# Optimization experiments

Hardware: AMD Instinct MI355X
Metric: run time of the kernel (lower is better)

The kernel has to match this reference:

```python
import jax, jax.numpy as jnp
import numpy as np

HEADS = 16
HIDDEN = 1024
DH = HIDDEN // HEADS
EPS = 1e-6


def setup_inputs() -> dict:
    key = jax.random.key(0)
    ks = jax.random.split(key, 18)
    B, S, D, H = 8, 4096, HIDDEN, HEADS
    std = 0.02
    inp = {
        "x": jax.random.normal(ks[0], (B, S, D), dtype=jnp.float32),
        "mask": jnp.zeros((B, 1, S), dtype=jnp.float32),
        "Wq": std * jax.random.normal(ks[1], (D, D), dtype=jnp.float32),
        "bq": jnp.zeros((D,), jnp.float32),
        "Wk": std * jax.random.normal(ks[2], (D, D), dtype=jnp.float32),
        "bk": jnp.zeros((D,), jnp.float32),
        "Wv": std * jax.random.normal(ks[3], (D, D), dtype=jnp.float32),
        "bv": jnp.zeros((D,), jnp.float32),
        "Wa": std * jax.random.normal(ks[4], (D, H), dtype=jnp.float32),
        "ba": jnp.zeros((H,), jnp.float32),
        "Wb": std * jax.random.normal(ks[5], (D, H), dtype=jnp.float32),
        "bb": jnp.zeros((H,), jnp.float32),
        "Wu": std * jax.random.normal(ks[6], (D, D), dtype=jnp.float32),
        "bu": jnp.zeros((D,), jnp.float32),
        "Wo": std * jax.random.normal(ks[7], (D, D), dtype=jnp.float32),
        "bo": jnp.zeros((D,), jnp.float32),
        "ln_g": jnp.ones((D,), jnp.float32),
        "ln_b": jnp.zeros((D,), jnp.float32),
    }
    return inp


def reference(x, mask, Wq, bq, Wk, bk, Wv, bv, Wa, ba, Wb, bb, Wu, bu, Wo, bo, ln_g, ln_b):
    B, S, D = x.shape
    H, dh = HEADS, D // HEADS
    scale = (D / H) ** -0.5

    q = x @ Wq + bq  # [B,S,D]
    k = x @ Wk + bk
    v = x @ Wv + bv

    # alpha pooling of q
    ascore = jnp.swapaxes((q @ Wa + ba) * scale, 1, 2) + mask  # [B,H,S]
    aw = jax.nn.softmax(ascore, axis=-1)
    qh = q.reshape(B, S, H, dh)
    q_av = jnp.einsum("bhs,bshd->bhd", aw, qh).reshape(B, 1, D)  # global query

    p = k * q_av  # [B,S,D], broadcast over seq

    # beta pooling of p
    bscore = jnp.swapaxes((p @ Wb + bb) * scale, 1, 2) + mask  # [B,H,S]
    bw = jax.nn.softmax(bscore, axis=-1)
    ph = p.reshape(B, S, H, dh)
    p_av = jnp.einsum("bhs,bshd->bhd", bw, ph).reshape(B, 1, D)  # global key

    u = p_av * v  # [B,S,D]
    r = u @ Wu + bu
    attn_out = (r + q) @ Wo + bo

    y = x + attn_out  # residual (dropout is identity at inference)
    mu = jnp.mean(y, axis=-1, keepdims=True)
    var = jnp.mean(jnp.square(y - mu), axis=-1, keepdims=True)
    return (y - mu) * jax.lax.rsqrt(var + EPS) * ln_g + ln_b
```

## Files before the change

kernel.cpp:

```cpp
#include <hip/hip_runtime.h>

typedef unsigned short u16;
typedef __bf16 bf16x8 __attribute__((ext_vector_type(8)));
typedef float  f32x4  __attribute__((ext_vector_type(4)));

__device__ __forceinline__ float b2f(u16 u) {
    unsigned int v = ((unsigned int)u) << 16;
    return __builtin_bit_cast(float, v);
}
__device__ __forceinline__ u16 f2b(float f) {
    unsigned int v = __builtin_bit_cast(unsigned int, f);
    v += 0x7fffu + ((v >> 16) & 1u);
    return (u16)(v >> 16);
}

#define GLD16(gp, lp) __builtin_amdgcn_global_load_lds( \
    (const __attribute__((address_space(1))) void*)(gp), \
    (__attribute__((address_space(3))) void*)(lp), 16, 0, 0)


__global__ __launch_bounds__(256) void convert_x(const float* __restrict__ x,
                                                 u16* __restrict__ xb) {
    size_t i = ((size_t)blockIdx.x * 256 + threadIdx.x) * 8;
    float4 v0 = *(const float4*)(x + i);
    float4 v1 = *(const float4*)(x + i + 4);
    ushort4 o0, o1;
    o0.x = f2b(v0.x); o0.y = f2b(v0.y); o0.z = f2b(v0.z); o0.w = f2b(v0.w);
    o1.x = f2b(v1.x); o1.y = f2b(v1.y); o1.z = f2b(v1.z); o1.w = f2b(v1.w);
    *(ushort4*)(xb + i)     = o0;
    *(ushort4*)(xb + i + 4) = o1;
}

__global__ __launch_bounds__(256)
void prep_all(const float* __restrict__ Wq, const float* __restrict__ Wk,
              const float* __restrict__ Wv, const float* __restrict__ Wo,
              u16* __restrict__ Wqkvt, u16* __restrict__ Wot,
              const float* __restrict__ Wa, u16* __restrict__ Wat,
              const float* __restrict__ bq, const float* __restrict__ bk,
              const float* __restrict__ bv, float* __restrict__ biasq) {
    __shared__ float tile[64][65];
    int blk = blockIdx.x;
    int tid = threadIdx.x;
    if (blk < 1024) {
        int g = blk >> 8;
        int lb = blk & 255;
        const float* W = (g == 0) ? Wq : (g == 1) ? Wk : (g == 2) ? Wv : Wo;
        u16* Wt = (g == 3) ? Wot : (Wqkvt + (size_t)g * 1048576);
        int kt = (lb & 15) * 64;
        int nt = (lb >> 4) * 64;
        int r = tid >> 4, c4 = (tid & 15) * 4;
        #pragma unroll
        for (int p = 0; p < 4; ++p) {
            int k = kt + p * 16 + r;
            float4 v = *(const float4*)(W + (size_t)k * 1024 + nt + c4);
            tile[c4 + 0][p * 16 + r] = v.x;
            tile[c4 + 1][p * 16 + r] = v.y;
            tile[c4 + 2][p * 16 + r] = v.z;
            tile[c4 + 3][p * 16 + r] = v.w;
        }
        __syncthreads();
        #pragma unroll
        for (int p = 0; p < 4; ++p) {
            int nl = p * 16 + r;
            ushort4 o;
            o.x = f2b(tile[nl][c4 + 0]); o.y = f2b(tile[nl][c4 + 1]);
            o.z = f2b(tile[nl][c4 + 2]); o.w = f2b(tile[nl][c4 + 3]);
            *(ushort4*)(Wt + (size_t)(nt + nl) * 1024 + kt + c4) = o;
        }
    } else if (blk < 1088) {
        int idx = (blk - 1024) * 256 + tid;
        int h = idx >> 10, k = idx & 1023;
        Wat[idx] = f2b(Wa[(k << 4) + h]);
    } else {
        int i = (blk - 1088) * 256 + tid;
        biasq[i] = (i < 1024) ? bq[i] : (i < 2048 ? bk[i - 1024] : bv[i - 2048]);
    }
}

__global__ __launch_bounds__(256) void wu_prime(const float* __restrict__ Wu,
                                                const float* __restrict__ p_av,
                                                u16* __restrict__ Wut) {
    __shared__ float tile[64][65];
    int kt = (blockIdx.x & 15) * 64;
    int nt = (blockIdx.x >> 4) * 64;
    int tid = threadIdx.x;
    int r = tid >> 4, c4 = (tid & 15) * 4;
    #pragma unroll
    for (int p = 0; p < 4; ++p) {
        int k = kt + p * 16 + r;
        float4 v = *(const float4*)(Wu + (size_t)k * 1024 + nt + c4);
        tile[c4 + 0][p * 16 + r] = v.x;
        tile[c4 + 1][p * 16 + r] = v.y;
        tile[c4 + 2][p * 16 + r] = v.z;
        tile[c4 + 3][p * 16 + r] = v.w;
    }
    __syncthreads();
    for (int b = 0; b < 8; ++b) {
        float4 pv = *(const float4*)(p_av + (size_t)b * 1024 + kt + c4);
        #pragma unroll
        for (int p = 0; p < 4; ++p) {
            int nl = p * 16 + r;
            ushort4 o;
            o.x = f2b(tile[nl][c4 + 0] * pv.x);
            o.y = f2b(tile[nl][c4 + 1] * pv.y);
            o.z = f2b(tile[nl][c4 + 2] * pv.z);
            o.w = f2b(tile[nl][c4 + 3] * pv.w);
            *(ushort4*)(Wut + ((size_t)b * 1024 + nt + nl) * 1024 + kt + c4) = o;
        }
    }
}

__global__ __launch_bounds__(256) void wbt_prep(const float* __restrict__ Wb,
                                                const float* __restrict__ q_av,
                                                u16* __restrict__ Wbt) {
    int idx = blockIdx.x * 256 + threadIdx.x;
    int b = idx >> 14, rem = idx & 16383;
    int h = rem >> 10, k = rem & 1023;
    Wbt[idx] = f2b(Wb[(k << 4) + h] * q_av[(b << 10) + k]);
}

__global__ __launch_bounds__(256, 4)
void gemm_bf16(const u16* __restrict__ A, int lda,
               const u16* __restrict__ Bt,
               const float* __restrict__ bias,
               const u16* __restrict__ addsrc, int ldadd,
               u16* __restrict__ C, int ldc,
               int N, int K, int batch_rows) {
    __shared__ u16 As[128 * 64];
    __shared__ u16 Bs[128 * 64];
    int ntiles = N >> 7;
    int bid = blockIdx.x;
    int mtiles = gridDim.x / ntiles;
    int tm, tn;
    if ((mtiles & 7) == 0) {
        int xcd = bid & 7, s = bid >> 3;
        int mper = mtiles >> 3;
        tm = xcd * mper + s / ntiles;
        tn = s - (s / ntiles) * ntiles;
    } else {
        tm = bid / ntiles; tn = bid - (bid / ntiles) * ntiles;
    }
    int m0 = tm << 7, n0 = tn << 7;
    if (batch_rows > 0) Bt += (size_t)(m0 / batch_rows) * (size_t)N * K;
    int tid = threadIdx.x, lane = tid & 63, w = tid >> 6;
    int wm = (w >> 1) << 6, wn = (w & 1) << 6;
    int quad = lane >> 4, l16 = lane & 15;
    int rph = l16 & 7;
    int lrow = lane >> 3;
    int lkg  = (lane & 7) ^ lrow;

    int idxA = (m0 + (w << 5) + lrow) * lda + (lkg << 3);
    int idxB = (n0 + (w << 5) + lrow) * K   + (lkg << 3);
    int stepA = lda << 3, stepB = K << 3;

    f32x4 zero = {0.f, 0.f, 0.f, 0.f};
    f32x4 acc[4][4];
    #pragma unroll
    for (int i = 0; i < 4; ++i)
        #pragma unroll
        for (int j = 0; j < 4; ++j) acc[i][j] = zero;

    for (int kt = 0; kt < K; kt += 64) {
        __syncthreads();
        #pragma unroll
        for (int j = 0; j < 4; ++j) {
            int c = (w << 2) + j;
            GLD16(A  + (idxA + j * stepA + kt), &As[c << 9]);
            GLD16(Bt + (idxB + j * stepB + kt), &Bs[c << 9]);
        }
        __syncthreads();
        #pragma unroll
        for (int kk = 0; kk < 2; ++kk) {
            bf16x8 a[4], b[4];
            int kg = (((kk << 2) + quad) ^ rph) << 3;
            #pragma unroll
            for (int i = 0; i < 4; ++i) {
                a[i] = *(const bf16x8*)&As[((wm + (i << 4) + l16) << 6) + kg];
                b[i] = *(const bf16x8*)&Bs[((wn + (i << 4) + l16) << 6) + kg];
            }
            #pragma unroll
            for (int mi = 0; mi < 4; ++mi)
                #pragma unroll
                for (int ni = 0; ni < 4; ++ni)
                    acc[mi][ni] = __builtin_amdgcn_mfma_f32_16x16x32_bf16(
                        a[mi], b[ni], acc[mi][ni], 0, 0, 0);
        }
    }
    #pragma unroll
    for (int mi = 0; mi < 4; ++mi) {
        #pragma unroll
        for (int ni = 0; ni < 4; ++ni) {
            int col = n0 + wn + (ni << 4) + l16;
            float bv = bias[col];
            #pragma unroll
            for (int rg = 0; rg < 4; ++rg) {
                int rowg = m0 + wm + (mi << 4) + (quad << 2) + rg;
                float vv = acc[mi][ni][rg] + bv;
                if (addsrc) vv += b2f(addsrc[(size_t)rowg * ldadd + col]);
                C[(size_t)rowg * ldc + col] = f2b(vv);
            }
        }
    }
}

__global__ __launch_bounds__(256)
void score_gemm(const u16* __restrict__ A, int lda,
                const u16* __restrict__ Bt,
                const float* __restrict__ bias16,
                const float* __restrict__ mask,
                float* __restrict__ outsc,
                float* __restrict__ pmax,
                int batched) {
    __shared__ u16 As[64 * 64];
    __shared__ u16 Bs[16 * 64];
    __shared__ float pm[16][16];
    int m0 = blockIdx.x << 6;
    int tid = threadIdx.x, lane = tid & 63, w = tid >> 6;
    int quad = lane >> 4, l16 = lane & 15;
    int rph = l16 & 7;
    int lrow = lane >> 3;
    int lkg  = (lane & 7) ^ lrow;
    const u16* Bb = Bt + (batched ? ((size_t)(m0 >> 12) << 14) : 0);

    int idxA = (m0 + (w << 4) + lrow) * lda + (lkg << 3);
    int stepA = lda << 3;
    int idxB = lrow * 1024 + (lkg << 3);

    f32x4 acc4 = (f32x4){0.f, 0.f, 0.f, 0.f};

    for (int kt = 0; kt < 1024; kt += 64) {
        __syncthreads();
        #pragma unroll
        for (int j = 0; j < 2; ++j) {
            int c = (w << 1) + j;
            GLD16(A + (idxA + j * stepA + kt), &As[c << 9]);
        }
        if (w < 2)
            GLD16(Bb + (idxB + w * 8192 + kt), &Bs[w << 9]);
        __syncthreads();
        #pragma unroll
        for (int kk = 0; kk < 2; ++kk) {
            int kg = (((kk << 2) + quad) ^ rph) << 3;
            bf16x8 b = *(const bf16x8*)&Bs[(l16 << 6) + kg];
            bf16x8 a = *(const bf16x8*)&As[(((w << 4) + l16) << 6) + kg];
            acc4 = __builtin_amdgcn_mfma_f32_16x16x32_bf16(a, b, acc4, 0, 0, 0);
        }
    }
    int bidx = m0 >> 12;
    float bv = bias16[l16];
    float* orow = outsc + (((size_t)bidx << 4) + l16) * 4096;
    const float* mrow = mask + ((size_t)bidx << 12);
    int sbase = (m0 & 4095) + (w << 4) + (quad << 2);
    float lm = -1e30f;
    #pragma unroll
    for (int rg = 0; rg < 4; ++rg) {
        float sv = 0.125f * (acc4[rg] + bv) + mrow[sbase + rg];
        orow[sbase + rg] = sv;
        lm = fmaxf(lm, sv);
    }
    pm[(w << 2) | quad][l16] = lm;
    __syncthreads();
    if (tid < 16) {
        float m = pm[0][tid];
        #pragma unroll
        for (int j = 1; j < 16; ++j) m = fmaxf(m, pm[j][tid]);
        pmax[(((bidx << 4) + tid) << 6) + (blockIdx.x & 63)] = m;
    }
}

__global__ __launch_bounds__(256)
void pool_sum(const float* __restrict__ score,
              const float* __restrict__ pmax,
              const u16* __restrict__ X, int ldx,
              float* __restrict__ part,
              float* __restrict__ parte) {
    __shared__ float psum[16][64];
    __shared__ float pes[16];
    __shared__ float smx;
    int blk = blockIdx.x, tid = threadIdx.x;
    int cc = blk & 7, bh = blk >> 3;
    int b = bh >> 4, h = bh & 15;
    if (tid < 64) {
        float m = pmax[(bh << 6) + tid];
        for (int o = 32; o; o >>= 1) m = fmaxf(m, __shfl_xor(m, o));
        if (tid == 0) smx = m;
    }
    __syncthreads();
    float mx = smx;
    const float* wrow = score + ((size_t)bh << 12) + (cc << 9);
    int dg = (tid & 15) << 2;
    int sc = tid >> 4;
    const u16* base = X + (size_t)((b << 12) + (cc << 9) + (sc << 5)) * ldx + (h << 6) + dg;
    float a0 = 0, a1 = 0, a2 = 0, a3 = 0, es = 0;
    for (int s = 0; s < 32; ++s) {
        float e = __expf(wrow[(sc << 5) + s] - mx);
        es += e;
        ushort4 uv = *(const ushort4*)(base + (size_t)s * ldx);
        a0 += e * b2f(uv.x); a1 += e * b2f(uv.y);
        a2 += e * b2f(uv.z); a3 += e * b2f(uv.w);
    }
    psum[sc][dg + 0] = a0; psum[sc][dg + 1] = a1;
    psum[sc][dg + 2] = a2; psum[sc][dg + 3] = a3;
    if ((tid & 15) == 0) pes[sc] = es;
    __syncthreads();
    if (tid < 64) {
        float t = 0.f;
        #pragma unroll
        for (int j = 0; j < 16; ++j) t += psum[j][tid];
        part[(((size_t)bh << 3) + cc) * 64 + tid] = t;
    }
    if (tid == 64) {
        float e = 0.f;
        #pragma unroll
        for (int j = 0; j < 16; ++j) e += pes[j];
        parte[(bh << 3) + cc] = e;
    }
}

__global__ __launch_bounds__(256)
void pool_finalize(const float* __restrict__ part,
                   const float* __restrict__ parte,
                   const float* __restrict__ mul,
                   float* __restrict__ outav) {
    int idx = blockIdx.x * 256 + threadIdx.x;
    int bh = idx >> 6;
    const float* p = part + ((size_t)bh << 9) + (idx & 63);
    const float* pe = parte + (bh << 3);
    float s = 0.f, e = 0.f;
    #pragma unroll
    for (int c = 0; c < 8; ++c) { s += p[c << 6]; e += pe[c]; }
    s /= e;
    if (mul) s *= mul[idx];
    outav[idx] = s;
}

__global__ __launch_bounds__(256)
void ln_kernel(const u16* __restrict__ Z, const float* __restrict__ g,
               const float* __restrict__ bta, float* __restrict__ outp) {
    __shared__ float rs1[4], rs2[4];
    int row = blockIdx.x, tid = threadIdx.x;
    const u16* zr = Z + ((size_t)row << 10);
    ushort4 uv = *(const ushort4*)(zr + (tid << 2));
    float v0 = b2f(uv.x), v1 = b2f(uv.y), v2 = b2f(uv.z), v3 = b2f(uv.w);
    float s = v0 + v1 + v2 + v3;
    float s2 = v0 * v0 + v1 * v1 + v2 * v2 + v3 * v3;
    for (int o = 32; o; o >>= 1) { s += __shfl_xor(s, o); s2 += __shfl_xor(s2, o); }
    if ((tid & 63) == 0) { rs1[tid >> 6] = s; rs2[tid >> 6] = s2; }
    __syncthreads();
    float S = rs1[0] + rs1[1] + rs1[2] + rs1[3];
    float S2 = rs2[0] + rs2[1] + rs2[2] + rs2[3];
    float mean = S * (1.0f / 1024.0f);
    float var = S2 * (1.0f / 1024.0f) - mean * mean;
    float inv = rsqrtf(var + 1e-6f);
    int c = tid << 2;
    float4 o4;
    o4.x = (v0 - mean) * inv * g[c + 0] + bta[c + 0];
    o4.y = (v1 - mean) * inv * g[c + 1] + bta[c + 1];
    o4.z = (v2 - mean) * inv * g[c + 2] + bta[c + 2];
    o4.w = (v3 - mean) * inv * g[c + 3] + bta[c + 3];
    *(float4*)(outp + ((size_t)row << 10) + c) = o4;
}


extern "C" void kernel_launch(void* const* d_in, const int* in_sizes, int n_in,
                              void* d_out, int out_size, void* d_ws, size_t ws_size,
                              hipStream_t stream) {
    (void)in_sizes; (void)n_in; (void)out_size;
    const float* x    = (const float*)d_in[0];
    const float* mask = (const float*)d_in[1];
    const float* Wq   = (const float*)d_in[2];
    const float* bq   = (const float*)d_in[3];
    const float* Wk   = (const float*)d_in[4];
    const float* bk   = (const float*)d_in[5];
    const float* Wv   = (const float*)d_in[6];
    const float* bv   = (const float*)d_in[7];
    const float* Wa   = (const float*)d_in[8];
    const float* ba   = (const float*)d_in[9];
    const float* Wb   = (const float*)d_in[10];
    const float* bb   = (const float*)d_in[11];
    const float* Wu   = (const float*)d_in[12];
    const float* bu   = (const float*)d_in[13];
    const float* Wo   = (const float*)d_in[14];
    const float* bo   = (const float*)d_in[15];
    const float* ln_g = (const float*)d_in[16];
    const float* ln_b = (const float*)d_in[17];
    float* outp = (float*)d_out;

    char* ws = (char*)d_ws;
    u16*   xb    = (u16*)(ws);
    u16*   qkv   = (u16*)(ws + 67108864);
    u16*   Wqkvt = (u16*)(ws + 268435456);
    u16*   Wot   = (u16*)(ws + 274726912);
    u16*   Wat   = (u16*)(ws + 276824064);
    u16*   Wbt   = (u16*)(ws + 276856832);
    float* score = (float*)(ws + 277118976);
    float* q_av  = (float*)(ws + 279216128);
    float* p_av  = (float*)(ws + 279248896);
    float* biasq = (float*)(ws + 279281664);
    u16*   Wubt  = (u16*)(ws + 279293952);
    float* part  = (float*)(ws + 296071168);
    float* pmax  = (float*)(ws + 296333312);
    float* parte = (float*)(ws + 296366080);
    if (ws_size < 296370176ULL) return;

    convert_x<<<16384, 256, 0, stream>>>(x, xb);
    prep_all<<<1100, 256, 0, stream>>>(Wq, Wk, Wv, Wo, Wqkvt, Wot, Wa, Wat,
                                       bq, bk, bv, biasq);

    gemm_bf16<<<6144, 256, 0, stream>>>(xb, 1024, Wqkvt, biasq,
                                        nullptr, 0, qkv, 3072, 3072, 1024, 0);
    score_gemm<<<512, 256, 0, stream>>>(qkv, 3072, Wat, ba, mask, score, pmax, 0);
    pool_sum<<<1024, 256, 0, stream>>>(score, pmax, qkv, 3072, part, parte);
    pool_finalize<<<32, 256, 0, stream>>>(part, parte, nullptr, q_av);
    wbt_prep<<<512, 256, 0, stream>>>(Wb, q_av, Wbt);
    score_gemm<<<512, 256, 0, stream>>>(qkv + 1024, 3072, Wbt, bb, mask, score, pmax, 1);
    pool_sum<<<1024, 256, 0, stream>>>(score, pmax, qkv + 1024, 3072, part, parte);
    pool_finalize<<<32, 256, 0, stream>>>(part, parte, q_av, p_av);
    wu_prime<<<256, 256, 0, stream>>>(Wu, p_av, Wubt);
    gemm_bf16<<<2048, 256, 0, stream>>>(qkv + 2048, 3072, Wubt, bu,
                                        qkv, 3072, qkv, 3072, 1024, 1024, 4096);
    gemm_bf16<<<2048, 256, 0, stream>>>(qkv, 3072, Wot, bo,
                                        xb, 1024, xb, 1024, 1024, 1024, 0);
    ln_kernel<<<32768, 256, 0, stream>>>(xb, ln_g, ln_b, outp);
}
```

Before: 836.0 us.

## Merge x conversion into prep kernel, swizzle GEMM tiles 2x2, batch epilogue loads

Folds the x fp32-to-bf16 conversion into the weight prep kernel so one launch does both. The GEMM tile mapping within each XCD becomes 2x2 blocked, which should improve L2 reuse of A and B tiles. The epilogue now loads all residual addsrc values for a row group before using them, so the loads can be in flight together instead of being serialized with the stores. The effect is small relative to the whole pipeline, and the bigger merged grid needs shared memory sized for the tile path even in conversion blocks, which may lower occupancy.

```diff
diff --git a/kernel.cpp b/kernel.cpp
--- a/kernel.cpp
+++ b/kernel.cpp
@@ -19,20 +19,9 @@
     (__attribute__((address_space(3))) void*)(lp), 16, 0, 0)
 
 
-__global__ __launch_bounds__(256) void convert_x(const float* __restrict__ x,
-                                                 u16* __restrict__ xb) {
-    size_t i = ((size_t)blockIdx.x * 256 + threadIdx.x) * 8;
-    float4 v0 = *(const float4*)(x + i);
-    float4 v1 = *(const float4*)(x + i + 4);
-    ushort4 o0, o1;
-    o0.x = f2b(v0.x); o0.y = f2b(v0.y); o0.z = f2b(v0.z); o0.w = f2b(v0.w);
-    o1.x = f2b(v1.x); o1.y = f2b(v1.y); o1.z = f2b(v1.z); o1.w = f2b(v1.w);
-    *(ushort4*)(xb + i)     = o0;
-    *(ushort4*)(xb + i + 4) = o1;
-}
-
 __global__ __launch_bounds__(256)
-void prep_all(const float* __restrict__ Wq, const float* __restrict__ Wk,
+void prep_all(const float* __restrict__ x, u16* __restrict__ xb,
+              const float* __restrict__ Wq, const float* __restrict__ Wk,
               const float* __restrict__ Wv, const float* __restrict__ Wo,
               u16* __restrict__ Wqkvt, u16* __restrict__ Wot,
               const float* __restrict__ Wa, u16* __restrict__ Wat,
@@ -41,9 +30,21 @@
     __shared__ float tile[64][65];
     int blk = blockIdx.x;
     int tid = threadIdx.x;
-    if (blk < 1024) {
-        int g = blk >> 8;
-        int lb = blk & 255;
+    if (blk < 16384) {
+        size_t i = ((size_t)blk * 256 + tid) * 8;
+        float4 v0 = *(const float4*)(x + i);
+        float4 v1 = *(const float4*)(x + i + 4);
+        ushort4 o0, o1;
+        o0.x = f2b(v0.x); o0.y = f2b(v0.y); o0.z = f2b(v0.z); o0.w = f2b(v0.w);
+        o1.x = f2b(v1.x); o1.y = f2b(v1.y); o1.z = f2b(v1.z); o1.w = f2b(v1.w);
+        *(ushort4*)(xb + i)     = o0;
+        *(ushort4*)(xb + i + 4) = o1;
+        return;
+    }
+    int wblk = blk - 16384;
+    if (wblk < 1024) {
+        int g = wblk >> 8;
+        int lb = wblk & 255;
         const float* W = (g == 0) ? Wq : (g == 1) ? Wk : (g == 2) ? Wv : Wo;
         u16* Wt = (g == 3) ? Wot : (Wqkvt + (size_t)g * 1048576);
         int kt = (lb & 15) * 64;
@@ -67,12 +68,12 @@
             o.z = f2b(tile[nl][c4 + 2]); o.w = f2b(tile[nl][c4 + 3]);
             *(ushort4*)(Wt + (size_t)(nt + nl) * 1024 + kt + c4) = o;
         }
-    } else if (blk < 1088) {
-        int idx = (blk - 1024) * 256 + tid;
+    } else if (wblk < 1088) {
+        int idx = (wblk - 1024) * 256 + tid;
         int h = idx >> 10, k = idx & 1023;
         Wat[idx] = f2b(Wa[(k << 4) + h]);
     } else {
-        int i = (blk - 1088) * 256 + tid;
+        int i = (wblk - 1088) * 256 + tid;
         biasq[i] = (i < 1024) ? bq[i] : (i < 2048 ? bk[i - 1024] : bv[i - 2048]);
     }
 }
@@ -135,8 +136,15 @@
     if ((mtiles & 7) == 0) {
         int xcd = bid & 7, s = bid >> 3;
         int mper = mtiles >> 3;
-        tm = xcd * mper + s / ntiles;
-        tn = s - (s / ntiles) * ntiles;
+        if (((mper | ntiles) & 1) == 0) {
+            int half = ntiles >> 1;
+            int sq = s >> 2, r = s & 3;
+            tm = xcd * mper + ((sq / half) << 1) + (r >> 1);
+            tn = ((sq - (sq / half) * half) << 1) + (r & 1);
+        } else {
+            tm = xcd * mper + s / ntiles;
+            tn = s - (s / ntiles) * ntiles;
+        }
     } else {
         tm = bid / ntiles; tn = bid - (bid / ntiles) * ntiles;
     }
@@ -188,6 +196,18 @@
     }
     #pragma unroll
     for (int mi = 0; mi < 4; ++mi) {
+        u16 av[4][4];
+        if (addsrc) {
+            #pragma unroll
+            for (int ni = 0; ni < 4; ++ni) {
+                int col = n0 + wn + (ni << 4) + l16;
+                #pragma unroll
+                for (int rg = 0; rg < 4; ++rg) {
+                    int rowg = m0 + wm + (mi << 4) + (quad << 2) + rg;
+                    av[ni][rg] = addsrc[(size_t)rowg * ldadd + col];
+                }
+            }
+        }
         #pragma unroll
         for (int ni = 0; ni < 4; ++ni) {
             int col = n0 + wn + (ni << 4) + l16;
@@ -196,7 +216,7 @@
             for (int rg = 0; rg < 4; ++rg) {
                 int rowg = m0 + wm + (mi << 4) + (quad << 2) + rg;
                 float vv = acc[mi][ni][rg] + bv;
-                if (addsrc) vv += b2f(addsrc[(size_t)rowg * ldadd + col]);
+                if (addsrc) vv += b2f(av[ni][rg]);
                 C[(size_t)rowg * ldc + col] = f2b(vv);
             }
         }
@@ -403,9 +423,8 @@
     float* parte = (float*)(ws + 296366080);
     if (ws_size < 296370176ULL) return;
 
-    convert_x<<<16384, 256, 0, stream>>>(x, xb);
-    prep_all<<<1100, 256, 0, stream>>>(Wq, Wk, Wv, Wo, Wqkvt, Wot, Wa, Wat,
-                                       bq, bk, bv, biasq);
+    prep_all<<<17484, 256, 0, stream>>>(x, xb, Wq, Wk, Wv, Wo, Wqkvt, Wot,
+                                        Wa, Wat, bq, bk, bv, biasq);
 
     gemm_bf16<<<6144, 256, 0, stream>>>(xb, 1024, Wqkvt, biasq,
                                         nullptr, 0, qkv, 3072, 3072, 1024, 0);
```

After: 763.2 us. 1.1x faster.
